# Kernel optimization log

Measured on AMD Instinct MI355X. Metric: run time of the kernel, lower is better.

Reference implementation:

```python
import jax, jax.numpy as jnp
import numpy as np

IN_FEATURES = 8192
OUT_FEATURES = 8192
CODESZ = 8            # E8 lattice dimension per code index
CODEBOOK_SIZE = 65536 # 2^16-entry codebook (16-bit indices)
TOKENS = 32           # decode-style batch


def fwht(x):
    """Fast Walsh-Hadamard transform (Sylvester order) along the last axis.
    n must be a power of 2. Unnormalized (multiply by H_n)."""
    n = x.shape[-1]
    steps = int(np.log2(n))
    h = 1
    for _ in range(steps):
        y = x.reshape(*x.shape[:-1], n // (2 * h), 2, h)
        a = y[..., 0, :]
        b = y[..., 1, :]
        x = jnp.stack([a + b, a - b], axis=-2).reshape(*y.shape[:-3], n)
        h *= 2
    return x


def setup_inputs() -> dict:
    key = jax.random.key(0)
    k0, k1, k2, k3, k4 = jax.random.split(key, 5)
    x = jax.random.normal(k0, (TOKENS, IN_FEATURES), dtype=jnp.float32)
    # learned codebook: CODEBOOK_SIZE vectors of CODESZ entries (E8P-like lattice points)
    codebook_table = jax.random.normal(k1, (CODEBOOK_SIZE, CODESZ), dtype=jnp.float32) * 0.1
    # quantized weight indices: [out_features, in_features // codesz]
    Qidxs = jax.random.randint(k2, (OUT_FEATURES, IN_FEATURES // CODESZ), 0, CODEBOOK_SIZE, dtype=jnp.int32)
    # random sign vectors (incoherence processing)
    SU = (2.0 * jax.random.randint(k3, (IN_FEATURES,), 0, 2) - 1.0).astype(jnp.float32)
    SV = (2.0 * jax.random.randint(k4, (OUT_FEATURES,), 0, 2) - 1.0).astype(jnp.float32)
    Wscale = jnp.array(0.02, dtype=jnp.float32)
    return {"x": x, "codebook_table": codebook_table, "Qidxs": Qidxs,
            "SU": SU, "SV": SV, "Wscale": Wscale}


def reference(x, codebook_table, Qidxs, SU, SV, Wscale):
    n_in = x.shape[-1]
    n_out = SV.shape[0]
    # input incoherence: sign flip then orthonormal Hadamard rotation (matmul_hadUt)
    xh = fwht(x * SU) * (1.0 / jnp.sqrt(jnp.float32(n_in)))  # [T, n_in]
    # codebook dequantization: gather lattice vectors and lay out as [n_out, n_in]
    W = codebook_table[Qidxs].reshape(n_out, n_in)
    # quantized matmul in the rotated basis
    z = xh @ W.T  # [T, n_out]
    # output rotation (matmul_hadU) + sign/scale (SV absorbs Wscale in the torch code)
    out = fwht(z) * (1.0 / jnp.sqrt(jnp.float32(n_out))) * (SV * Wscale)
    return out
```

## Files before the change

### kernel.cpp

```cpp
#include <hip/hip_runtime.h>
#include <hip/hip_bf16.h>


typedef __attribute__((ext_vector_type(4))) float f32x4;
typedef __attribute__((ext_vector_type(8))) __bf16 bf16x8;
typedef __attribute__((ext_vector_type(4))) __bf16 bf16x4;
typedef __attribute__((ext_vector_type(4))) int i32x4;

#define IN_F 8192
#define OUT_F 8192
#define TOKENS 32
#define KSPLIT 8
#define INV_SQRT_8192 0.011048543456039806f
#define PAD(i) ((i) + ((i) >> 5))

__device__ inline void fwht32_reg(float* r) {
    #pragma unroll
    for (int h = 1; h < 32; h <<= 1)
        #pragma unroll
        for (int i = 0; i < 32; i += 2 * h)
            #pragma unroll
            for (int j = 0; j < h; ++j) {
                float a = r[i + j], b = r[i + j + h];
                r[i + j] = a + b;
                r[i + j + h] = a - b;
            }
}

__device__ inline void fwht8192_lds(float* s, int tid) {
    float r[32];
    int b1 = tid * 32;
    #pragma unroll
    for (int j = 0; j < 32; ++j) r[j] = s[PAD(b1 + j)];
    fwht32_reg(r);
    #pragma unroll
    for (int j = 0; j < 32; ++j) s[PAD(b1 + j)] = r[j];
    __syncthreads();
    int b2 = (tid & 31) + (tid >> 5) * 1024;
    #pragma unroll
    for (int j = 0; j < 32; ++j) r[j] = s[PAD(b2 + 32 * j)];
    fwht32_reg(r);
    #pragma unroll
    for (int j = 0; j < 32; ++j) s[PAD(b2 + 32 * j)] = r[j];
    __syncthreads();
    #pragma unroll
    for (int jj = 0; jj < 4; ++jj) {
        float g[8];
        int b3 = tid * 4 + jj;
        #pragma unroll
        for (int k = 0; k < 8; ++k) g[k] = s[PAD(b3 + 1024 * k)];
        #pragma unroll
        for (int h = 1; h < 8; h <<= 1)
            #pragma unroll
            for (int i = 0; i < 8; i += 2 * h)
                #pragma unroll
                for (int j = 0; j < h; ++j) {
                    float a = g[i + j], b = g[i + j + h];
                    g[i + j] = a + b;
                    g[i + j + h] = a - b;
                }
        #pragma unroll
        for (int k = 0; k < 8; ++k) s[PAD(b3 + 1024 * k)] = g[k];
    }
    __syncthreads();
}

__global__ __launch_bounds__(256)
void prep_kernel(const float* __restrict__ cb, __bf16* __restrict__ cbb,
                 const float* __restrict__ x, const float* __restrict__ su,
                 __bf16* __restrict__ xh) {
    __shared__ float s[8192 + 256];
    const int tid = threadIdx.x;
    if (blockIdx.x < 512) {
        int i = blockIdx.x * 256 + tid;
        float4 v = ((const float4*)cb)[i];
        bf16x4 o;
        o[0] = (__bf16)v.x; o[1] = (__bf16)v.y;
        o[2] = (__bf16)v.z; o[3] = (__bf16)v.w;
        ((bf16x4*)cbb)[i] = o;
        return;
    }
    const int t = blockIdx.x - 512;
    #pragma unroll
    for (int i = tid; i < IN_F; i += 256)
        s[PAD(i)] = x[t * IN_F + i] * su[i];
    __syncthreads();
    fwht8192_lds(s, tid);
    #pragma unroll
    for (int i = tid; i < IN_F; i += 256)
        xh[t * IN_F + i] = (__bf16)(s[PAD(i)] * INV_SQRT_8192);
}

__global__ __launch_bounds__(512, 4)
void qgemm_kernel(const int* __restrict__ qidxs,
                  const __bf16* __restrict__ cb,
                  const __bf16* __restrict__ xh,
                  float* __restrict__ zpart) {
    __shared__ __align__(16) __bf16 xt[32 * 1024];
    const int ks = blockIdx.x & 7;
    const int nb = blockIdx.x >> 3;
    const int tid = threadIdx.x;
    const int wave = tid >> 6, lane = tid & 63;
    const int quad = lane >> 4, l16 = lane & 15;
    const int n = nb * 128 + wave * 16 + l16;
    const int* qrow = qidxs + (size_t)n * 1024 + ks * 128;
    const bf16x8* cbv = (const bf16x8*)cb;

    #pragma unroll
    for (int i = 0; i < 8; ++i) {
        int f = i * 512 + tid, r = f >> 7, c = f & 127;
        i32x4 v = *(const i32x4*)(xh + (size_t)r * IN_F + ks * 1024 + c * 8);
        *(i32x4*)(xt + ((r * 128 + (c ^ (r & 7))) << 3)) = v;
    }
    __syncthreads();

    f32x4 acc0 = {0.f, 0.f, 0.f, 0.f};
    f32x4 acc1 = {0.f, 0.f, 0.f, 0.f};
    int idx[8][4];
    bf16x8 bfr[8][4];

    #pragma unroll
    for (int g = 0; g < 4; ++g)
        #pragma unroll
        for (int j = 0; j < 4; ++j)
            idx[g][j] = qrow[(g * 4 + j) * 4 + quad];
    #pragma unroll
    for (int g = 0; g < 3; ++g)
        #pragma unroll
        for (int j = 0; j < 4; ++j)
            bfr[g][j] = cbv[idx[g][j]];

    #pragma unroll
    for (int g = 0; g < 8; ++g) {
        if (g + 4 < 8) {
            #pragma unroll
            for (int j = 0; j < 4; ++j)
                idx[g + 4][j] = qrow[((g + 4) * 4 + j) * 4 + quad];
        }
        if (g + 3 < 8) {
            #pragma unroll
            for (int j = 0; j < 4; ++j)
                bfr[g + 3][j] = cbv[idx[g + 3][j]];
        }
        #pragma unroll
        for (int j = 0; j < 4; ++j) {
            const int T = g * 4 + j;
            const int sw = (((4 * T + quad) ^ (l16 & 7)) << 3);
            bf16x8 a0 = *(const bf16x8*)(xt + l16 * 1024 + sw);
            bf16x8 a1 = *(const bf16x8*)(xt + (l16 + 16) * 1024 + sw);
            acc0 = __builtin_amdgcn_mfma_f32_16x16x32_bf16(a0, bfr[g][j], acc0, 0, 0, 0);
            acc1 = __builtin_amdgcn_mfma_f32_16x16x32_bf16(a1, bfr[g][j], acc1, 0, 0, 0);
        }
    }

    float* zp = zpart + (size_t)ks * TOKENS * OUT_F + n;
    #pragma unroll
    for (int r = 0; r < 4; ++r) {
        zp[(quad * 4 + r) * OUT_F] = acc0[r];
        zp[(16 + quad * 4 + r) * OUT_F] = acc1[r];
    }
}

__global__ __launch_bounds__(256)
void zsumA_kernel(const float* __restrict__ zpart, float* __restrict__ ztmp) {
    __shared__ float s[1024 + 32];
    const int t = blockIdx.x >> 3, ch = blockIdx.x & 7, tid = threadIdx.x;
    const float* zb = zpart + (size_t)t * OUT_F + ch * 1024 + tid * 4;
    float4 a = {0.f, 0.f, 0.f, 0.f};
    #pragma unroll
    for (int k = 0; k < KSPLIT; ++k) {
        float4 v = *(const float4*)(zb + (size_t)k * TOKENS * OUT_F);
        a.x += v.x; a.y += v.y; a.z += v.z; a.w += v.w;
    }
    s[PAD(4 * tid + 0)] = a.x; s[PAD(4 * tid + 1)] = a.y;
    s[PAD(4 * tid + 2)] = a.z; s[PAD(4 * tid + 3)] = a.w;
    __syncthreads();
    for (int h = 1; h < 256; h <<= 1) {
        #pragma unroll
        for (int b = 0; b < 2; ++b) {
            int p = tid + b * 256;
            int g = p >> 7, off = p & 127;
            int i0 = g * 256 + (((off & ~(h - 1)) << 1) | (off & (h - 1)));
            float A = s[PAD(i0)], B = s[PAD(i0 + h)];
            s[PAD(i0)] = A + B; s[PAD(i0 + h)] = A - B;
        }
        __syncthreads();
    }
    float4 o;
    o.x = s[PAD(4 * tid + 0)]; o.y = s[PAD(4 * tid + 1)];
    o.z = s[PAD(4 * tid + 2)]; o.w = s[PAD(4 * tid + 3)];
    *(float4*)(ztmp + (size_t)t * OUT_F + ch * 1024 + tid * 4) = o;
}

__global__ __launch_bounds__(256)
void zsumB_kernel(const float* __restrict__ ztmp, const float* __restrict__ sv,
                  const float* __restrict__ wscale, float* __restrict__ out) {
    const int t = blockIdx.x;
    const int jl = threadIdx.x;
    float r[32];
    #pragma unroll
    for (int jh = 0; jh < 32; ++jh)
        r[jh] = ztmp[(size_t)t * OUT_F + jh * 256 + jl];
    fwht32_reg(r);
    const float sc = INV_SQRT_8192 * wscale[0];
    #pragma unroll
    for (int jh = 0; jh < 32; ++jh)
        out[(size_t)t * OUT_F + jh * 256 + jl] = r[jh] * sc * sv[jh * 256 + jl];
}

extern "C" void kernel_launch(void* const* d_in, const int* in_sizes, int n_in,
                              void* d_out, int out_size, void* d_ws, size_t ws_size,
                              hipStream_t stream) {
    const float* x      = (const float*)d_in[0];
    const float* cb     = (const float*)d_in[1];
    const int*   qidxs  = (const int*)d_in[2];
    const float* su     = (const float*)d_in[3];
    const float* sv     = (const float*)d_in[4];
    const float* wscale = (const float*)d_in[5];
    float* out = (float*)d_out;

    char* ws = (char*)d_ws;
    __bf16* cb_bf16 = (__bf16*)ws;
    __bf16* xh      = (__bf16*)(ws + (1u << 20));
    float*  zpart   = (float*)(ws + (1u << 20) + (512u << 10));
    float*  ztmp    = (float*)ws;

    hipLaunchKernelGGL(prep_kernel, dim3(544), dim3(256), 0, stream,
                       cb, cb_bf16, x, su, xh);
    hipLaunchKernelGGL(qgemm_kernel, dim3(64 * KSPLIT), dim3(512), 0, stream,
                       qidxs, cb_bf16, xh, zpart);
    hipLaunchKernelGGL(zsumA_kernel, dim3(256), dim3(256), 0, stream,
                       zpart, ztmp);
    hipLaunchKernelGGL(zsumB_kernel, dim3(TOKENS), dim3(256), 0, stream,
                       ztmp, sv, wscale, out);
}
```

Baseline: 139.1 us.

## Double K-split with atomic accumulation and drop partial-sum buffer reads

Raises the K-split from 8 to 16 with half-size K chunks per block, doubling the grid and raising the occupancy hint so more blocks are resident to hide codebook gather latency. Partial results are accumulated with float atomics into one zeroed buffer instead of writing 8 partial slabs that the reduction kernel then re-reads. Qidxs loads become nontemporal. The cost is an extra memset and atomic contention, and the floating-point summation order becomes nondeterministic.

```diff
diff --git a/kernel.cpp b/kernel.cpp
--- a/kernel.cpp
+++ b/kernel.cpp
@@ -10,7 +10,8 @@
 #define IN_F 8192
 #define OUT_F 8192
 #define TOKENS 32
-#define KSPLIT 8
+#define KSPLIT 16
+#define KCHUNK 512
 #define INV_SQRT_8192 0.011048543456039806f
 #define PAD(i) ((i) + ((i) >> 5))
 
@@ -91,87 +92,82 @@
         xh[t * IN_F + i] = (__bf16)(s[PAD(i)] * INV_SQRT_8192);
 }
 
-__global__ __launch_bounds__(512, 4)
+__global__ __launch_bounds__(512, 8)
 void qgemm_kernel(const int* __restrict__ qidxs,
                   const __bf16* __restrict__ cb,
                   const __bf16* __restrict__ xh,
-                  float* __restrict__ zpart) {
-    __shared__ __align__(16) __bf16 xt[32 * 1024];
-    const int ks = blockIdx.x & 7;
-    const int nb = blockIdx.x >> 3;
+                  float* __restrict__ z) {
+    __shared__ __align__(16) __bf16 xt[32 * KCHUNK];
+    const int ks = blockIdx.x & 15;
+    const int nb = blockIdx.x >> 4;
     const int tid = threadIdx.x;
     const int wave = tid >> 6, lane = tid & 63;
     const int quad = lane >> 4, l16 = lane & 15;
     const int n = nb * 128 + wave * 16 + l16;
-    const int* qrow = qidxs + (size_t)n * 1024 + ks * 128;
+    const int* qrow = qidxs + (size_t)n * 1024 + ks * (KCHUNK / 8);
     const bf16x8* cbv = (const bf16x8*)cb;
 
     #pragma unroll
-    for (int i = 0; i < 8; ++i) {
-        int f = i * 512 + tid, r = f >> 7, c = f & 127;
-        i32x4 v = *(const i32x4*)(xh + (size_t)r * IN_F + ks * 1024 + c * 8);
-        *(i32x4*)(xt + ((r * 128 + (c ^ (r & 7))) << 3)) = v;
+    for (int i = 0; i < 4; ++i) {
+        int f = i * 512 + tid, r = f >> 6, c = f & 63;
+        i32x4 v = *(const i32x4*)(xh + (size_t)r * IN_F + ks * KCHUNK + c * 8);
+        *(i32x4*)(xt + ((r * 64 + (c ^ (r & 7))) << 3)) = v;
     }
     __syncthreads();
 
     f32x4 acc0 = {0.f, 0.f, 0.f, 0.f};
     f32x4 acc1 = {0.f, 0.f, 0.f, 0.f};
-    int idx[8][4];
-    bf16x8 bfr[8][4];
-
-    #pragma unroll
-    for (int g = 0; g < 4; ++g)
+    int idx[4][4];
+    bf16x8 bfr[4][4];
+
+    #pragma unroll
+    for (int g = 0; g < 3; ++g)
         #pragma unroll
         for (int j = 0; j < 4; ++j)
-            idx[g][j] = qrow[(g * 4 + j) * 4 + quad];
-    #pragma unroll
-    for (int g = 0; g < 3; ++g)
+            idx[g][j] = __builtin_nontemporal_load(qrow + (g * 4 + j) * 4 + quad);
+    #pragma unroll
+    for (int g = 0; g < 2; ++g)
         #pragma unroll
         for (int j = 0; j < 4; ++j)
             bfr[g][j] = cbv[idx[g][j]];
 
     #pragma unroll
-    for (int g = 0; g < 8; ++g) {
-        if (g + 4 < 8) {
+    for (int g = 0; g < 4; ++g) {
+        if (g + 3 < 4) {
             #pragma unroll
             for (int j = 0; j < 4; ++j)
-                idx[g + 4][j] = qrow[((g + 4) * 4 + j) * 4 + quad];
-        }
-        if (g + 3 < 8) {
+                idx[g + 3][j] =
+                    __builtin_nontemporal_load(qrow + ((g + 3) * 4 + j) * 4 + quad);
+        }
+        if (g + 2 < 4) {
             #pragma unroll
             for (int j = 0; j < 4; ++j)
-                bfr[g + 3][j] = cbv[idx[g + 3][j]];
+                bfr[g + 2][j] = cbv[idx[g + 2][j]];
         }
         #pragma unroll
         for (int j = 0; j < 4; ++j) {
             const int T = g * 4 + j;
-            const int sw = (((4 * T + quad) ^ (l16 & 7)) << 3);
-            bf16x8 a0 = *(const bf16x8*)(xt + l16 * 1024 + sw);
-            bf16x8 a1 = *(const bf16x8*)(xt + (l16 + 16) * 1024 + sw);
+            const int sw = (((T * 4 + quad) ^ (l16 & 7)) << 3);
+            bf16x8 a0 = *(const bf16x8*)(xt + l16 * KCHUNK + sw);
+            bf16x8 a1 = *(const bf16x8*)(xt + (l16 + 16) * KCHUNK + sw);
             acc0 = __builtin_amdgcn_mfma_f32_16x16x32_bf16(a0, bfr[g][j], acc0, 0, 0, 0);
             acc1 = __builtin_amdgcn_mfma_f32_16x16x32_bf16(a1, bfr[g][j], acc1, 0, 0, 0);
         }
     }
 
-    float* zp = zpart + (size_t)ks * TOKENS * OUT_F + n;
+    float* zp = z + n;
     #pragma unroll
     for (int r = 0; r < 4; ++r) {
-        zp[(quad * 4 + r) * OUT_F] = acc0[r];
-        zp[(16 + quad * 4 + r) * OUT_F] = acc1[r];
+        unsafeAtomicAdd(zp + (quad * 4 + r) * OUT_F, acc0[r]);
+        unsafeAtomicAdd(zp + (16 + quad * 4 + r) * OUT_F, acc1[r]);
     }
 }
 
 __global__ __launch_bounds__(256)
-void zsumA_kernel(const float* __restrict__ zpart, float* __restrict__ ztmp) {
+void zsumA_kernel(const float* __restrict__ z, float* __restrict__ ztmp) {
     __shared__ float s[1024 + 32];
     const int t = blockIdx.x >> 3, ch = blockIdx.x & 7, tid = threadIdx.x;
-    const float* zb = zpart + (size_t)t * OUT_F + ch * 1024 + tid * 4;
-    float4 a = {0.f, 0.f, 0.f, 0.f};
-    #pragma unroll
-    for (int k = 0; k < KSPLIT; ++k) {
-        float4 v = *(const float4*)(zb + (size_t)k * TOKENS * OUT_F);
-        a.x += v.x; a.y += v.y; a.z += v.z; a.w += v.w;
-    }
+    float4 a = *(const float4*)(z + (size_t)t * OUT_F + ch * 1024 + tid * 4);
     s[PAD(4 * tid + 0)] = a.x; s[PAD(4 * tid + 1)] = a.y;
     s[PAD(4 * tid + 2)] = a.z; s[PAD(4 * tid + 3)] = a.w;
     __syncthreads();
@@ -222,15 +218,16 @@
     char* ws = (char*)d_ws;
     __bf16* cb_bf16 = (__bf16*)ws;
     __bf16* xh      = (__bf16*)(ws + (1u << 20));
-    float*  zpart   = (float*)(ws + (1u << 20) + (512u << 10));
-    float*  ztmp    = (float*)ws;
-
+    float*  zbuf    = (float*)(ws + (1u << 20) + (512u << 10));
+    float*  ztmp    = (float*)(ws + (1u << 20) + (512u << 10) + (1u << 20));
+
+    hipMemsetAsync(zbuf, 0, (size_t)TOKENS * OUT_F * 4, stream);
     hipLaunchKernelGGL(prep_kernel, dim3(544), dim3(256), 0, stream,
                        cb, cb_bf16, x, su, xh);
     hipLaunchKernelGGL(qgemm_kernel, dim3(64 * KSPLIT), dim3(512), 0, stream,
-                       qidxs, cb_bf16, xh, zpart);
+                       qidxs, cb_bf16, xh, zbuf);
     hipLaunchKernelGGL(zsumA_kernel, dim3(256), dim3(256), 0, stream,
-                       zpart, ztmp);
+                       zbuf, ztmp);
     hipLaunchKernelGGL(zsumB_kernel, dim3(TOKENS), dim3(256), 0, stream,
                        ztmp, sv, wscale, out);
 }
```

After: 171.0 us. 1.23x slower.
